# Optimization experiments

Measured on AMD Instinct MI355X. Metric: run time of the kernel, lower is better.

The kernel has to match this reference:

```python
import jax, jax.numpy as jnp
import numpy as np

N_NODES = 50000
N_EDGES = 800000
IN_DIM = 64
EDGE_DIM = 32
OUT_DIM = 64
HID = IN_DIM + EDGE_DIM  # repo MLP defaults hidden width = layer input width


def setup_inputs() -> dict:
    key = jax.random.key(0)
    ks = jax.random.split(key, 7)
    x = jax.random.normal(ks[0], (N_NODES, IN_DIM), dtype=jnp.float32)
    edge_index = jax.random.randint(ks[1], (2, N_EDGES), 0, N_NODES, dtype=jnp.int64)
    edge_attr = jax.random.normal(ks[2], (N_EDGES, EDGE_DIM), dtype=jnp.float32)
    s1 = 1.0 / np.sqrt(HID)
    s2 = 1.0 / np.sqrt(HID)
    W1 = jax.random.normal(ks[3], (HID, HID), dtype=jnp.float32) * s1
    b1 = jnp.zeros((HID,), dtype=jnp.float32)
    W2 = jax.random.normal(ks[4], (HID, OUT_DIM), dtype=jnp.float32) * s2
    b2 = jnp.zeros((OUT_DIM,), dtype=jnp.float32)
    return {"x": x, "edge_index": edge_index, "edge_attr": edge_attr,
            "W1": W1, "b1": b1, "W2": W2, "b2": b2}


def reference(x, edge_index, edge_attr, W1, b1, W2, b2):
    row, col = edge_index[0], edge_index[1]
    n_nodes = x.shape[0]
    # gather source node features and fuse with edge features: [E, IN+EDGE]
    h = jnp.concatenate([x[row], edge_attr], axis=1)
    # MLP: one hidden layer with ReLU, linear output
    h = jax.nn.relu(h @ W1 + b1)
    h = h @ W2 + b2  # [E, OUT_DIM]
    # scatter_mean over destination (col) indices
    summed = jax.ops.segment_sum(h, col, num_segments=n_nodes)  # [N, OUT_DIM]
    counts = jax.ops.segment_sum(jnp.ones((h.shape[0],), dtype=h.dtype), col,
                                 num_segments=n_nodes)
    return summed / jnp.maximum(counts, 1.0)[:, None]
```

## Files before the change

kernel.cpp:

```cpp
#include <hip/hip_runtime.h>

#define N_EDGES  800000
#define N_NODES  50000
#define IN_DIM   64
#define EDGE_DIM 32
#define HID      96
#define OUT_DIM  64
#define BE       128
#define PAD      104
#define NTILES   (N_EDGES / BE)
#define THREADS  512
#define GRID     512
#define SCAN_B   1024
#define SCAN_NB  ((N_NODES + SCAN_B - 1) / SCAN_B)

typedef __attribute__((ext_vector_type(8))) short  short8;
typedef __attribute__((ext_vector_type(4))) ushort bf16x4;
typedef __attribute__((ext_vector_type(4))) float  f32x4;

__device__ inline ushort f2bf(float f) {
    union { float f; unsigned u; } v; v.f = f;
    unsigned r = v.u + 0x7FFFu + ((v.u >> 16) & 1u);
    return (ushort)(r >> 16);
}
__device__ inline float b2f(ushort u) {
    union { unsigned u; float f; } v; v.u = ((unsigned)u) << 16;
    return v.f;
}

__global__ __launch_bounds__(256) void zero_hist_kernel(int* __restrict__ hist) {
    int i = blockIdx.x * 256 + threadIdx.x;
    if (i < N_NODES) hist[i] = 0;
}

__global__ __launch_bounds__(256) void hist_kernel(const int* __restrict__ ei,
                                                   int* __restrict__ hist) {
    int e = blockIdx.x * 256 + threadIdx.x;
    if (e < N_EDGES) atomicAdd(&hist[ei[N_EDGES + e]], 1);
}

__global__ __launch_bounds__(SCAN_B) void scan1_kernel(const int* __restrict__ hist,
                                                       int* __restrict__ starts,
                                                       int* __restrict__ bsums) {
    __shared__ int buf[2][SCAN_B];
    const int tid = threadIdx.x;
    const int gid = blockIdx.x * SCAN_B + tid;
    int v = (gid < N_NODES) ? hist[gid] : 0;
    int cur = 0;
    buf[0][tid] = v;
    __syncthreads();
    #pragma unroll
    for (int off = 1; off < SCAN_B; off <<= 1) {
        int t = buf[cur][tid] + ((tid >= off) ? buf[cur][tid - off] : 0);
        buf[cur ^ 1][tid] = t;
        __syncthreads();
        cur ^= 1;
    }
    int incl = buf[cur][tid];
    if (gid < N_NODES) starts[gid] = incl;
    if (tid == SCAN_B - 1) bsums[blockIdx.x] = incl;
}

__global__ __launch_bounds__(64) void scan2_kernel(int* __restrict__ bsums) {
    if (threadIdx.x == 0) {
        int acc = 0;
        for (int i = 0; i < SCAN_NB; ++i) { int t = bsums[i]; bsums[i] = acc; acc += t; }
    }
}

__global__ __launch_bounds__(SCAN_B) void scan3_kernel(const int* __restrict__ hist,
                                                       int* __restrict__ starts,
                                                       int* __restrict__ cursor,
                                                       const int* __restrict__ bsums) {
    const int gid = blockIdx.x * SCAN_B + threadIdx.x;
    if (gid < N_NODES) {
        int e = starts[gid] - hist[gid] + bsums[blockIdx.x];
        starts[gid] = e;
        cursor[gid] = e;
    }
}

__global__ __launch_bounds__(256) void fill_kernel(const int* __restrict__ ei,
                                                   int* __restrict__ cursor,
                                                   int* __restrict__ ids) {
    int e = blockIdx.x * 256 + threadIdx.x;
    if (e < N_EDGES) {
        int c = ei[N_EDGES + e];
        int p = atomicAdd(&cursor[c], 1);
        ids[p] = e;
    }
}

__global__ __launch_bounds__(256) void zero_kernel(float* __restrict__ out,
                                                   float* __restrict__ cnt) {
    int i = blockIdx.x * 256 + threadIdx.x;
    if (i < N_NODES * OUT_DIM) out[i] = 0.0f;
    if (i < N_NODES) cnt[i] = 0.0f;
}

__global__ __launch_bounds__(256) void div_kernel(float* __restrict__ out,
                                                  const float* __restrict__ cnt) {
    int i = blockIdx.x * 256 + threadIdx.x;
    if (i < N_NODES * OUT_DIM) {
        float c = cnt[i / OUT_DIM];
        out[i] = out[i] / fmaxf(c, 1.0f);
    }
}

template <bool ATOMIC>
__global__ __launch_bounds__(THREADS, 4) void edge_mlp_mfma_kernel(
    const float* __restrict__ x,
    const int*   __restrict__ ei,
    const float* __restrict__ ea,
    const float* __restrict__ W1,
    const float* __restrict__ b1,
    const float* __restrict__ W2,
    const float* __restrict__ b2,
    float*       __restrict__ out,
    float*       __restrict__ cnt,
    ushort*      __restrict__ temp)
{
    __shared__ ushort sA[BE][PAD];
    __shared__ ushort sW1T[HID][PAD];
    __shared__ ushort sW2T[OUT_DIM][PAD];

    const int tid  = threadIdx.x;
    const int wave = tid >> 6;
    const int lane = tid & 63;
    const int lr   = lane & 15;
    const int lg   = lane >> 4;
    const int el_base = wave * 16;

    #pragma unroll 2
    for (int i = tid; i < HID * HID / 4; i += THREADS) {
        float4 v = reinterpret_cast<const float4*>(W1)[i];
        int k = (i * 4) / HID, n = (i * 4) % HID;
        sW1T[n + 0][k] = f2bf(v.x); sW1T[n + 1][k] = f2bf(v.y);
        sW1T[n + 2][k] = f2bf(v.z); sW1T[n + 3][k] = f2bf(v.w);
    }
    #pragma unroll 2
    for (int i = tid; i < HID * OUT_DIM / 4; i += THREADS) {
        float4 v = reinterpret_cast<const float4*>(W2)[i];
        int k = (i * 4) / OUT_DIM, n = (i * 4) % OUT_DIM;
        sW2T[n + 0][k] = f2bf(v.x); sW2T[n + 1][k] = f2bf(v.y);
        sW2T[n + 2][k] = f2bf(v.z); sW2T[n + 3][k] = f2bf(v.w);
    }
    float rb1[6], rb2[4];
    #pragma unroll
    for (int nt = 0; nt < 6; ++nt) rb1[nt] = b1[nt * 16 + lr];
    #pragma unroll
    for (int nt = 0; nt < 4; ++nt) rb2[nt] = b2[nt * 16 + lr];
    __syncthreads();

    for (int tl = blockIdx.x; tl < NTILES; tl += gridDim.x) {
        const int e0 = tl * BE;

        {
            const int el   = el_base + (lane >> 2);
            const int part = lane & 3;
            const int e    = e0 + el;
            const int src  = ei[e];
            const float4* xp = reinterpret_cast<const float4*>(x) + (size_t)src * 16;
            const float4* ep = reinterpret_cast<const float4*>(ea) + (size_t)e * 8;
            #pragma unroll
            for (int i = 0; i < 6; ++i) {
                const int f = part + 4 * i;
                float4 v = (i < 4) ? xp[f] : ep[f - 16];
                bf16x4 w = { f2bf(v.x), f2bf(v.y), f2bf(v.z), f2bf(v.w) };
                *(bf16x4*)&sA[el][f * 4] = w;
            }
            if constexpr (ATOMIC) {
                if (part == 0) atomicAdd(cnt + ei[N_EDGES + e], 1.0f);
            }
        }
        asm volatile("s_waitcnt lgkmcnt(0)" ::: "memory");
        __builtin_amdgcn_sched_barrier(0);

        short8 af[3];
        #pragma unroll
        for (int ks = 0; ks < 3; ++ks)
            af[ks] = *(const short8*)&sA[el_base + lr][ks * 32 + lg * 8];

        f32x4 acc1[6];
        #pragma unroll
        for (int nt = 0; nt < 6; ++nt) {
            float bv = rb1[nt];
            acc1[nt] = f32x4{ bv, bv, bv, bv };
        }
        #pragma unroll
        for (int nt = 0; nt < 6; ++nt) {
            short8 bf[3];
            #pragma unroll
            for (int ks = 0; ks < 3; ++ks)
                bf[ks] = *(const short8*)&sW1T[nt * 16 + lr][ks * 32 + lg * 8];
            #pragma unroll
            for (int ks = 0; ks < 3; ++ks)
                acc1[nt] = __builtin_amdgcn_mfma_f32_16x16x32_bf16(
                    af[ks], bf[ks], acc1[nt], 0, 0, 0);
        }

        #pragma unroll
        for (int nt = 0; nt < 6; ++nt)
            #pragma unroll
            for (int j = 0; j < 4; ++j)
                sA[el_base + lg * 4 + j][nt * 16 + lr] =
                    f2bf(fmaxf(acc1[nt][j], 0.0f));
        asm volatile("s_waitcnt lgkmcnt(0)" ::: "memory");
        __builtin_amdgcn_sched_barrier(0);

        short8 a2[3];
        #pragma unroll
        for (int ks = 0; ks < 3; ++ks)
            a2[ks] = *(const short8*)&sA[el_base + lr][ks * 32 + lg * 8];

        f32x4 acc2[4];
        #pragma unroll
        for (int nt = 0; nt < 4; ++nt) {
            float bv = rb2[nt];
            acc2[nt] = f32x4{ bv, bv, bv, bv };
        }
        #pragma unroll
        for (int nt = 0; nt < 4; ++nt) {
            short8 bf[3];
            #pragma unroll
            for (int ks = 0; ks < 3; ++ks)
                bf[ks] = *(const short8*)&sW2T[nt * 16 + lr][ks * 32 + lg * 8];
            #pragma unroll
            for (int ks = 0; ks < 3; ++ks)
                acc2[nt] = __builtin_amdgcn_mfma_f32_16x16x32_bf16(
                    a2[ks], bf[ks], acc2[nt], 0, 0, 0);
        }

        if constexpr (ATOMIC) {
            int nd[4];
            #pragma unroll
            for (int j = 0; j < 4; ++j)
                nd[j] = ei[N_EDGES + e0 + el_base + lg * 4 + j];
            #pragma unroll
            for (int nt = 0; nt < 4; ++nt)
                #pragma unroll
                for (int j = 0; j < 4; ++j)
                    atomicAdd(out + (size_t)nd[j] * OUT_DIM + nt * 16 + lr,
                              acc2[nt][j]);
        } else {
            #pragma unroll
            for (int nt = 0; nt < 4; ++nt)
                #pragma unroll
                for (int j = 0; j < 4; ++j)
                    sA[el_base + lg * 4 + j][nt * 16 + lr] = f2bf(acc2[nt][j]);
            asm volatile("s_waitcnt lgkmcnt(0)" ::: "memory");
            __builtin_amdgcn_sched_barrier(0);
            const int rr = lane >> 2, pp = lane & 3;
            ushort* dst = temp + (size_t)(e0 + el_base + rr) * OUT_DIM + pp * 16;
            short8 v0 = *(const short8*)&sA[el_base + rr][pp * 16];
            short8 v1 = *(const short8*)&sA[el_base + rr][pp * 16 + 8];
            *(short8*)dst = v0;
            *(short8*)(dst + 8) = v1;
        }
    }
}

__global__ __launch_bounds__(256) void pull_kernel(const ushort* __restrict__ temp,
                                                   const int* __restrict__ ids,
                                                   const int* __restrict__ starts,
                                                   const int* __restrict__ hist,
                                                   float* __restrict__ out) {
    const int wave = threadIdx.x >> 6;
    const int lane = threadIdx.x & 63;
    const int node = blockIdx.x * 4 + wave;
    if (node >= N_NODES) return;
    const int deg = hist[node];
    const int st  = starts[node];
    float s = 0.0f;
    int i = 0;
    for (; i + 4 <= deg; i += 4) {
        int e0 = ids[st + i], e1 = ids[st + i + 1];
        int e2 = ids[st + i + 2], e3 = ids[st + i + 3];
        float a = b2f(temp[(size_t)e0 * OUT_DIM + lane]);
        float b = b2f(temp[(size_t)e1 * OUT_DIM + lane]);
        float c = b2f(temp[(size_t)e2 * OUT_DIM + lane]);
        float d = b2f(temp[(size_t)e3 * OUT_DIM + lane]);
        s += (a + b) + (c + d);
    }
    for (; i < deg; ++i)
        s += b2f(temp[(size_t)ids[st + i] * OUT_DIM + lane]);
    out[(size_t)node * OUT_DIM + lane] = s / fmaxf((float)deg, 1.0f);
}

extern "C" void kernel_launch(void* const* d_in, const int* in_sizes, int n_in,
                              void* d_out, int out_size, void* d_ws, size_t ws_size,
                              hipStream_t stream) {
    const float* x  = (const float*)d_in[0];
    const int*   ei = (const int*)d_in[1];
    const float* ea = (const float*)d_in[2];
    const float* W1 = (const float*)d_in[3];
    const float* b1 = (const float*)d_in[4];
    const float* W2 = (const float*)d_in[5];
    const float* b2 = (const float*)d_in[6];
    float* out = (float*)d_out;

    char* ws = (char*)d_ws;
    const size_t tempB    = (size_t)N_EDGES * OUT_DIM * sizeof(ushort);
    const size_t idsOff   = tempB;
    const size_t histOff  = idsOff + (size_t)N_EDGES * 4;
    const size_t strOff   = histOff + (size_t)N_NODES * 4;
    const size_t curOff   = strOff + (size_t)N_NODES * 4;
    const size_t bsumOff  = curOff + (size_t)N_NODES * 4;
    const size_t need     = bsumOff + 64 * 4;

    if (ws_size >= need) {
        ushort* temp  = (ushort*)ws;
        int* ids      = (int*)(ws + idsOff);
        int* hist     = (int*)(ws + histOff);
        int* starts   = (int*)(ws + strOff);
        int* cursor   = (int*)(ws + curOff);
        int* bsums    = (int*)(ws + bsumOff);

        zero_hist_kernel<<<(N_NODES + 255) / 256, 256, 0, stream>>>(hist);
        hist_kernel<<<N_EDGES / 256, 256, 0, stream>>>(ei, hist);
        scan1_kernel<<<SCAN_NB, SCAN_B, 0, stream>>>(hist, starts, bsums);
        scan2_kernel<<<1, 64, 0, stream>>>(bsums);
        scan3_kernel<<<SCAN_NB, SCAN_B, 0, stream>>>(hist, starts, cursor, bsums);
        fill_kernel<<<N_EDGES / 256, 256, 0, stream>>>(ei, cursor, ids);
        edge_mlp_mfma_kernel<false><<<GRID, THREADS, 0, stream>>>(
            x, ei, ea, W1, b1, W2, b2, out, nullptr, temp);
        pull_kernel<<<(N_NODES + 3) / 4, 256, 0, stream>>>(temp, ids, starts, hist, out);
    } else {
        float* cnt = (float*)d_ws;
        zero_kernel<<<(N_NODES * OUT_DIM + 255) / 256, 256, 0, stream>>>(out, cnt);
        edge_mlp_mfma_kernel<true><<<GRID, THREADS, 0, stream>>>(
            x, ei, ea, W1, b1, W2, b2, out, cnt, nullptr);
        div_kernel<<<(N_NODES * OUT_DIM + 255) / 256, 256, 0, stream>>>(out, cnt);
    }
}
```

Before: 204.0 us.

## Write edge MLP outputs in destination-sorted order, prefetch next tile, merge scan kernels

The fill kernel now records each edge's sorted slot (epos) rather than a list of edge ids. The MLP kernel writes its bf16 output row directly to that slot, so the pull kernel reads each node's edges contiguously with vector loads instead of gathering through ids. The MLP loop also prefetches the next tile's gathered x and edge_attr into registers while the current tile computes, which raises register pressure. The single-thread scan2 kernel is folded into scan3 as a wave reduction, and the hist zeroing kernel becomes a hipMemsetAsync.

```diff
diff --git a/kernel.cpp b/kernel.cpp
--- a/kernel.cpp
+++ b/kernel.cpp
@@ -26,11 +26,6 @@
 __device__ inline float b2f(ushort u) {
     union { unsigned u; float f; } v; v.u = ((unsigned)u) << 16;
     return v.f;
-}
-
-__global__ __launch_bounds__(256) void zero_hist_kernel(int* __restrict__ hist) {
-    int i = blockIdx.x * 256 + threadIdx.x;
-    if (i < N_NODES) hist[i] = 0;
 }
 
 __global__ __launch_bounds__(256) void hist_kernel(const int* __restrict__ ei,
@@ -61,20 +56,21 @@
     if (tid == SCAN_B - 1) bsums[blockIdx.x] = incl;
 }
 
-__global__ __launch_bounds__(64) void scan2_kernel(int* __restrict__ bsums) {
-    if (threadIdx.x == 0) {
-        int acc = 0;
-        for (int i = 0; i < SCAN_NB; ++i) { int t = bsums[i]; bsums[i] = acc; acc += t; }
-    }
-}
-
 __global__ __launch_bounds__(SCAN_B) void scan3_kernel(const int* __restrict__ hist,
                                                        int* __restrict__ starts,
                                                        int* __restrict__ cursor,
                                                        const int* __restrict__ bsums) {
+    __shared__ int s_off;
+    if (threadIdx.x < 64) {
+        int v = ((int)threadIdx.x < (int)blockIdx.x) ? bsums[threadIdx.x] : 0;
+        #pragma unroll
+        for (int o = 32; o >= 1; o >>= 1) v += __shfl_xor(v, o, 64);
+        if (threadIdx.x == 0) s_off = v;
+    }
+    __syncthreads();
     const int gid = blockIdx.x * SCAN_B + threadIdx.x;
     if (gid < N_NODES) {
-        int e = starts[gid] - hist[gid] + bsums[blockIdx.x];
+        int e = starts[gid] - hist[gid] + s_off;
         starts[gid] = e;
         cursor[gid] = e;
     }
@@ -82,12 +78,12 @@
 
 __global__ __launch_bounds__(256) void fill_kernel(const int* __restrict__ ei,
                                                    int* __restrict__ cursor,
-                                                   int* __restrict__ ids) {
+                                                   int* __restrict__ epos) {
     int e = blockIdx.x * 256 + threadIdx.x;
     if (e < N_EDGES) {
         int c = ei[N_EDGES + e];
         int p = atomicAdd(&cursor[c], 1);
-        ids[p] = e;
+        epos[e] = p;
     }
 }
 
@@ -118,7 +114,8 @@
     const float* __restrict__ b2,
     float*       __restrict__ out,
     float*       __restrict__ cnt,
-    ushort*      __restrict__ temp)
+    ushort*      __restrict__ temp,
+    const int*   __restrict__ epos)
 {
     __shared__ ushort sA[BE][PAD];
     __shared__ ushort sW1T[HID][PAD];
@@ -130,6 +127,8 @@
     const int lr   = lane & 15;
     const int lg   = lane >> 4;
     const int el_base = wave * 16;
+    const int el   = el_base + (lane >> 2);
+    const int part = lane & 3;
 
     #pragma unroll 2
     for (int i = tid; i < HID * HID / 4; i += THREADS) {
@@ -152,27 +151,56 @@
     for (int nt = 0; nt < 4; ++nt) rb2[nt] = b2[nt * 16 + lr];
     __syncthreads();
 
-    for (int tl = blockIdx.x; tl < NTILES; tl += gridDim.x) {
-        const int e0 = tl * BE;
-
+    float4 px0, px1, px2, px3, pe0, pe1;
+    int ppos = 0, pdst = 0;
+    int tl = blockIdx.x;
+    {
+        const int e = tl * BE + el;
+        const int src = ei[e];
+        if constexpr (ATOMIC) pdst = ei[N_EDGES + e];
+        else                  ppos = epos[e];
+        const float4* xp = reinterpret_cast<const float4*>(x) + (size_t)src * 16;
+        const float4* ep = reinterpret_cast<const float4*>(ea) + (size_t)e * 8;
+        px0 = xp[part]; px1 = xp[part + 4]; px2 = xp[part + 8]; px3 = xp[part + 12];
+        pe0 = ep[part]; pe1 = ep[part + 4];
+    }
+
+    for (; tl < NTILES; tl += GRID) {
         {
-            const int el   = el_base + (lane >> 2);
-            const int part = lane & 3;
-            const int e    = e0 + el;
-            const int src  = ei[e];
+            bf16x4 w;
+            w = bf16x4{ f2bf(px0.x), f2bf(px0.y), f2bf(px0.z), f2bf(px0.w) };
+            *(bf16x4*)&sA[el][(part +  0) * 4] = w;
+            w = bf16x4{ f2bf(px1.x), f2bf(px1.y), f2bf(px1.z), f2bf(px1.w) };
+            *(bf16x4*)&sA[el][(part +  4) * 4] = w;
+            w = bf16x4{ f2bf(px2.x), f2bf(px2.y), f2bf(px2.z), f2bf(px2.w) };
+            *(bf16x4*)&sA[el][(part +  8) * 4] = w;
+            w = bf16x4{ f2bf(px3.x), f2bf(px3.y), f2bf(px3.z), f2bf(px3.w) };
+            *(bf16x4*)&sA[el][(part + 12) * 4] = w;
+            w = bf16x4{ f2bf(pe0.x), f2bf(pe0.y), f2bf(pe0.z), f2bf(pe0.w) };
+            *(bf16x4*)&sA[el][(part + 16) * 4] = w;
+            w = bf16x4{ f2bf(pe1.x), f2bf(pe1.y), f2bf(pe1.z), f2bf(pe1.w) };
+            *(bf16x4*)&sA[el][(part + 20) * 4] = w;
+        }
+        const int cpos = ppos, cdst = pdst;
+        if constexpr (ATOMIC) {
+            if (part == 0) atomicAdd(cnt + cdst, 1.0f);
+        }
+
+        const int tn = tl + GRID;
+        const bool have = (tn < NTILES);
+        float4 nx0, nx1, nx2, nx3, ne0, ne1;
+        int npos = 0, ndst = 0;
+        if (have) {
+            const int e = tn * BE + el;
+            const int src = ei[e];
+            if constexpr (ATOMIC) ndst = ei[N_EDGES + e];
+            else                  npos = epos[e];
             const float4* xp = reinterpret_cast<const float4*>(x) + (size_t)src * 16;
             const float4* ep = reinterpret_cast<const float4*>(ea) + (size_t)e * 8;
-            #pragma unroll
-            for (int i = 0; i < 6; ++i) {
-                const int f = part + 4 * i;
-                float4 v = (i < 4) ? xp[f] : ep[f - 16];
-                bf16x4 w = { f2bf(v.x), f2bf(v.y), f2bf(v.z), f2bf(v.w) };
-                *(bf16x4*)&sA[el][f * 4] = w;
-            }
-            if constexpr (ATOMIC) {
-                if (part == 0) atomicAdd(cnt + ei[N_EDGES + e], 1.0f);
-            }
-        }
+            nx0 = xp[part]; nx1 = xp[part + 4]; nx2 = xp[part + 8]; nx3 = xp[part + 12];
+            ne0 = ep[part]; ne1 = ep[part + 4];
+        }
+
         asm volatile("s_waitcnt lgkmcnt(0)" ::: "memory");
         __builtin_amdgcn_sched_barrier(0);
 
@@ -235,7 +263,7 @@
             int nd[4];
             #pragma unroll
             for (int j = 0; j < 4; ++j)
-                nd[j] = ei[N_EDGES + e0 + el_base + lg * 4 + j];
+                nd[j] = ei[N_EDGES + tl * BE + el_base + lg * 4 + j];
             #pragma unroll
             for (int nt = 0; nt < 4; ++nt)
                 #pragma unroll
@@ -250,18 +278,22 @@
                     sA[el_base + lg * 4 + j][nt * 16 + lr] = f2bf(acc2[nt][j]);
             asm volatile("s_waitcnt lgkmcnt(0)" ::: "memory");
             __builtin_amdgcn_sched_barrier(0);
-            const int rr = lane >> 2, pp = lane & 3;
-            ushort* dst = temp + (size_t)(e0 + el_base + rr) * OUT_DIM + pp * 16;
-            short8 v0 = *(const short8*)&sA[el_base + rr][pp * 16];
-            short8 v1 = *(const short8*)&sA[el_base + rr][pp * 16 + 8];
+            ushort* dst = temp + (size_t)cpos * OUT_DIM + part * 16;
+            short8 v0 = *(const short8*)&sA[el][part * 16];
+            short8 v1 = *(const short8*)&sA[el][part * 16 + 8];
             *(short8*)dst = v0;
             *(short8*)(dst + 8) = v1;
         }
+
+        if (have) {
+            px0 = nx0; px1 = nx1; px2 = nx2; px3 = nx3;
+            pe0 = ne0; pe1 = ne1;
+            ppos = npos; pdst = ndst;
+        }
     }
 }
 
 __global__ __launch_bounds__(256) void pull_kernel(const ushort* __restrict__ temp,
-                                                   const int* __restrict__ ids,
                                                    const int* __restrict__ starts,
                                                    const int* __restrict__ hist,
                                                    float* __restrict__ out) {
@@ -271,20 +303,29 @@
     if (node >= N_NODES) return;
     const int deg = hist[node];
     const int st  = starts[node];
-    float s = 0.0f;
-    int i = 0;
-    for (; i + 4 <= deg; i += 4) {
-        int e0 = ids[st + i], e1 = ids[st + i + 1];
-        int e2 = ids[st + i + 2], e3 = ids[st + i + 3];
-        float a = b2f(temp[(size_t)e0 * OUT_DIM + lane]);
-        float b = b2f(temp[(size_t)e1 * OUT_DIM + lane]);
-        float c = b2f(temp[(size_t)e2 * OUT_DIM + lane]);
-        float d = b2f(temp[(size_t)e3 * OUT_DIM + lane]);
-        s += (a + b) + (c + d);
-    }
-    for (; i < deg; ++i)
-        s += b2f(temp[(size_t)ids[st + i] * OUT_DIM + lane]);
-    out[(size_t)node * OUT_DIM + lane] = s / fmaxf((float)deg, 1.0f);
+    const int r   = lane >> 4;
+    const int g   = lane & 15;
+    float sx = 0.f, sy = 0.f, sz = 0.f, sw = 0.f;
+    const uint2* base = reinterpret_cast<const uint2*>(temp) + (size_t)st * 16 + g;
+    for (int i = r; i < deg; i += 4) {
+        uint2 u = base[(size_t)i * 16];
+        sx += b2f((ushort)(u.x & 0xFFFFu));
+        sy += b2f((ushort)(u.x >> 16));
+        sz += b2f((ushort)(u.y & 0xFFFFu));
+        sw += b2f((ushort)(u.y >> 16));
+    }
+    #pragma unroll
+    for (int o = 16; o <= 32; o <<= 1) {
+        sx += __shfl_xor(sx, o, 64);
+        sy += __shfl_xor(sy, o, 64);
+        sz += __shfl_xor(sz, o, 64);
+        sw += __shfl_xor(sw, o, 64);
+    }
+    if (r == 0) {
+        float inv = 1.0f / fmaxf((float)deg, 1.0f);
+        float4 o4 = { sx * inv, sy * inv, sz * inv, sw * inv };
+        *reinterpret_cast<float4*>(out + (size_t)node * OUT_DIM + g * 4) = o4;
+    }
 }
 
 extern "C" void kernel_launch(void* const* d_in, const int* in_sizes, int n_in,
@@ -301,8 +342,8 @@
 
     char* ws = (char*)d_ws;
     const size_t tempB    = (size_t)N_EDGES * OUT_DIM * sizeof(ushort);
-    const size_t idsOff   = tempB;
-    const size_t histOff  = idsOff + (size_t)N_EDGES * 4;
+    const size_t eposOff  = tempB;
+    const size_t histOff  = eposOff + (size_t)N_EDGES * 4;
     const size_t strOff   = histOff + (size_t)N_NODES * 4;
     const size_t curOff   = strOff + (size_t)N_NODES * 4;
     const size_t bsumOff  = curOff + (size_t)N_NODES * 4;
@@ -310,26 +351,25 @@
 
     if (ws_size >= need) {
         ushort* temp  = (ushort*)ws;
-        int* ids      = (int*)(ws + idsOff);
+        int* epos     = (int*)(ws + eposOff);
         int* hist     = (int*)(ws + histOff);
         int* starts   = (int*)(ws + strOff);
         int* cursor   = (int*)(ws + curOff);
         int* bsums    = (int*)(ws + bsumOff);
 
-        zero_hist_kernel<<<(N_NODES + 255) / 256, 256, 0, stream>>>(hist);
+        hipMemsetAsync(hist, 0, (size_t)N_NODES * 4, stream);
         hist_kernel<<<N_EDGES / 256, 256, 0, stream>>>(ei, hist);
         scan1_kernel<<<SCAN_NB, SCAN_B, 0, stream>>>(hist, starts, bsums);
-        scan2_kernel<<<1, 64, 0, stream>>>(bsums);
         scan3_kernel<<<SCAN_NB, SCAN_B, 0, stream>>>(hist, starts, cursor, bsums);
-        fill_kernel<<<N_EDGES / 256, 256, 0, stream>>>(ei, cursor, ids);
+        fill_kernel<<<N_EDGES / 256, 256, 0, stream>>>(ei, cursor, epos);
         edge_mlp_mfma_kernel<false><<<GRID, THREADS, 0, stream>>>(
-            x, ei, ea, W1, b1, W2, b2, out, nullptr, temp);
-        pull_kernel<<<(N_NODES + 3) / 4, 256, 0, stream>>>(temp, ids, starts, hist, out);
+            x, ei, ea, W1, b1, W2, b2, out, nullptr, temp, epos);
+        pull_kernel<<<(N_NODES + 3) / 4, 256, 0, stream>>>(temp, starts, hist, out);
     } else {
         float* cnt = (float*)d_ws;
         zero_kernel<<<(N_NODES * OUT_DIM + 255) / 256, 256, 0, stream>>>(out, cnt);
         edge_mlp_mfma_kernel<true><<<GRID, THREADS, 0, stream>>>(
-            x, ei, ea, W1, b1, W2, b2, out, cnt, nullptr);
+            x, ei, ea, W1, b1, W2, b2, out, cnt, nullptr, nullptr);
         div_kernel<<<(N_NODES * OUT_DIM + 255) / 256, 256, 0, stream>>>(out, cnt);
     }
 }
```

Result: faster. 174.3 us, median of 2 (-14.6%).
